# Kernel optimization log

Hardware: AMD Instinct MI355X
Metric: run time of the kernel (lower is better)

Reference implementation:

```python
import jax, jax.numpy as jnp
import numpy as np

S_CONST = float(np.log(9.0))   # self.s = log(9)
K = 1.0                        # soft_sign sharpness (config.k)
RHO = 1.0
ALPHA0 = 0.01
BETA0 = 0.1
DECAY = 0.99


def soft_sign(x, k=K):
    # E2Efold soft sign: sigmoid(2*k*x)
    return jax.nn.sigmoid(2.0 * k * x)


def constraint_matrix(x):
    # x: [B, L, 4] -> m: [B, L, L]; pairing constraint AU+CG+UG outer products,
    # symmetrized, with |i-j|<=3 band zeroed (diags mask in torch version).
    base_a, base_u, base_c, base_g = x[..., 0], x[..., 1], x[..., 2], x[..., 3]

    def sym_outer(p, q):
        m = p[:, :, None] * q[:, None, :]
        return m + jnp.swapaxes(m, -1, -2)

    m = sym_outer(base_a, base_u) + sym_outer(base_c, base_g) + sym_outer(base_u, base_g)
    L = x.shape[1]
    i = jnp.arange(L)
    band = jnp.abs(i[:, None] - i[None, :]) <= 3  # [L, L] bool
    return jnp.where(band, jnp.zeros((), m.dtype), m)


def contact_a(a_hat, m):
    a = a_hat * a_hat
    a = (a + jnp.swapaxes(a, -1, -2)) * 0.5
    return a * m


def setup_inputs() -> dict:
    key = jax.random.key(0)
    k1, k2 = jax.random.split(key)
    B, L = 16, 512
    u = jax.random.normal(k1, (B, L, L), jnp.float32) * 2.0
    x = jax.random.uniform(k2, (B, L, 4), jnp.float32)
    return {"u": u, "x": x, "timesteps": 20}


def reference(u, x, timesteps):
    m = constraint_matrix(x)
    u = soft_sign(u - S_CONST) * u
    a_hat = jax.nn.sigmoid(u) * jax.lax.stop_gradient(soft_sign(u - S_CONST))
    a = contact_a(a_hat, m)
    lmbd = jax.lax.stop_gradient(jax.nn.relu(jnp.sum(a, -1) - 1.0))

    # per-step decayed learning rates: step t uses alpha0*decay^t (for grad step)
    # and alpha0*decay^(t+1) for the soft-threshold (torch decays alpha in between)
    t_idx = jnp.arange(timesteps, dtype=jnp.float32)
    alphas = ALPHA0 * DECAY ** t_idx
    betas = BETA0 * DECAY ** t_idx

    def step(carry, ab):
        lmbd, a, a_hat = carry
        alpha, beta = ab
        grad_a = -u / 2.0 + (lmbd * soft_sign(jnp.sum(a, -1) - 1.0))[..., None]
        grad = a_hat * m * (grad_a + jnp.swapaxes(grad_a, -1, -2))
        a_hat_new = a_hat - alpha * grad
        a_hat_new = jax.nn.relu(jnp.abs(a_hat_new) - RHO * alpha * DECAY)
        a_hat_new = jnp.clip(a_hat_new, -1.0, 1.0)
        a_new = contact_a(a_hat_new, m)
        lmbd_new = lmbd + beta * jax.nn.relu(jnp.sum(a_new, -1) - 1.0)
        return (lmbd_new, a_new, a_hat_new), a_new

    _, a_stack = jax.lax.scan(step, (lmbd, a, a_hat), (alphas, betas))
    return a_stack  # [timesteps, B, L, L] == a_t_list[1:]
```

## Files before the change

### kernel.cpp

```cpp
#include <hip/hip_runtime.h>
#include <math.h>

#define BB 16
#define LL 512
#define TS 20
#define TT 64
#define NT (LL / TT)
#define NPAIR (NT * (NT + 1) / 2)
#define NUNIT 32
#define NBLK (BB * NUNIT)
#define BLL (BB * LL * LL)
#define NROW (BB * LL)
#define RSPSTEP (BB * NT * LL)
#define PADI 32

#define S_CONST 2.19722457733621938f

__device__ __forceinline__ float sgm(float v) { return 1.0f / (1.0f + __expf(-v)); }
__device__ __forceinline__ float ahat_of(float up) {
  return sgm(up) * sgm(2.0f * (up - S_CONST));
}

__device__ __forceinline__ void st_agent(float* p, float v) {
  __hip_atomic_store(p, v, __ATOMIC_RELAXED, __HIP_MEMORY_SCOPE_AGENT);
}
__device__ __forceinline__ float ld_agent(const float* p) {
  return __hip_atomic_load(p, __ATOMIC_RELAXED, __HIP_MEMORY_SCOPE_AGENT);
}
__device__ __forceinline__ void bump(int* p) {
  __hip_atomic_fetch_add(p, 1, __ATOMIC_RELAXED, __HIP_MEMORY_SCOPE_AGENT);
}
__device__ __forceinline__ void spin_ge(const int* p, int target) {
  while (__hip_atomic_load(p, __ATOMIC_RELAXED, __HIP_MEMORY_SCOPE_AGENT) < target) {
    __builtin_amdgcn_s_sleep(1);
  }
  asm volatile("" ::: "memory");
}

__device__ __forceinline__ void decode_unit(int p, int& RI, int& RJ, bool& dg) {
  if (p < 28) {
    int base = 0, i = 0;
    while (p >= base + (NT - 1 - i)) { base += NT - 1 - i; ++i; }
    RI = i;
    RJ = i + 1 + (p - base);
    dg = false;
  } else {
    int g = p - 28;
    RI = 2 * g;
    RJ = 2 * g + 1;
    dg = true;
  }
}

__global__ __launch_bounds__(256, 2) void k_fused(const float* __restrict__ u,
                                                  const float* __restrict__ x,
                                                  float* __restrict__ rsp,
                                                  int* __restrict__ arr,
                                                  float* __restrict__ out) {
  __shared__ float t1[TT][TT + 1];
  __shared__ float t2[TT][TT + 1];
  __shared__ float xr[2][TT][4];
  __shared__ float xt[2][TT][4];
  __shared__ float cI[TT];
  __shared__ float cJ[TT];

  int b = blockIdx.x / NUNIT;
  int p = blockIdx.x % NUNIT;
  int RI, RJ;
  bool dg;
  decode_unit(p, RI, RJ, dg);
  int C1 = dg ? RI : RJ;
  int C2 = dg ? RJ : RI;

  int tid = threadIdx.x;
  int tx = tid & 15, ty = tid >> 4;

  int* ctrI = &arr[(b * NT + RI) * PADI];
  int* ctrJ = &arr[(b * NT + RJ) * PADI];

  if (tid < 128) {
    int which = tid >> 6;
    int r = tid & 63;
    int gi = (which ? RJ : RI) * TT + r;
    const float* xp = x + ((b * LL) + gi) * 4;
    float A = xp[0], U = xp[1], C = xp[2], G = xp[3];
    xr[which][r][0] = A; xr[which][r][1] = U; xr[which][r][2] = C; xr[which][r][3] = G;
    xt[which][r][0] = U; xt[which][r][1] = A + G; xt[which][r][2] = G; xt[which][r][3] = C + U;
  }

  int lrow = 0;
  if (tid < 128) {
    int which = tid >> 6;
    int r = tid & 63;
    lrow = (which ? RJ : RI) * TT + r;
  }
  float lmbd = 0.0f;

  float av1[4][4], av2[4][4];
  float wv1[4][4], wv2[4][4];
  float mv1[4][4], mv2[4][4];

  __syncthreads();

#pragma unroll
  for (int k = 0; k < 4; ++k) {
    int r = ty + 16 * k;
    {
      int i = RI * TT + r;
      int off = (b * LL + i) * LL + C1 * TT + 4 * tx;
      float4 u4 = *reinterpret_cast<const float4*>(u + off);
      float uu[4] = {u4.x, u4.y, u4.z, u4.w};
#pragma unroll
      for (int q = 0; q < 4; ++q) {
        float up = sgm(2.0f * (uu[q] - S_CONST)) * uu[q];
        t1[r][4 * tx + q] = up;
        av1[k][q] = ahat_of(up);
      }
    }
    {
      int i = RJ * TT + r;
      int off = (b * LL + i) * LL + C2 * TT + 4 * tx;
      float4 u4 = *reinterpret_cast<const float4*>(u + off);
      float uu[4] = {u4.x, u4.y, u4.z, u4.w};
#pragma unroll
      for (int q = 0; q < 4; ++q) {
        float up = sgm(2.0f * (uu[q] - S_CONST)) * uu[q];
        t2[r][4 * tx + q] = up;
        av2[k][q] = ahat_of(up);
      }
    }
  }
  __syncthreads();

  {
    float (*T1)[TT + 1] = dg ? t1 : t2;
    float (*T2)[TT + 1] = dg ? t2 : t1;
    float (*xc1)[4] = dg ? xt[0] : xt[1];
    float (*xc2)[4] = dg ? xt[1] : xt[0];
    float* rsp0 = rsp;

#pragma unroll
    for (int k = 0; k < 4; ++k) {
      int r = ty + 16 * k;
      {
        int i = RI * TT + r;
        float rs = 0.0f;
#pragma unroll
        for (int q = 0; q < 4; ++q) {
          int c = 4 * tx + q;
          int j = C1 * TT + c;
          float upT = T1[c][r];
          wv1[k][q] = -0.5f * (t1[r][c] + upT);
          int d = i - j; d = d < 0 ? -d : d;
          float mm = (d <= 3) ? 0.0f
                              : xr[0][r][0] * xc1[c][0] + xr[0][r][1] * xc1[c][1] +
                                    xr[0][r][2] * xc1[c][2] + xr[0][r][3] * xc1[c][3];
          mv1[k][q] = mm;
          float aT = ahat_of(upT);
          float a = av1[k][q];
          rs += 0.5f * (a * a + aT * aT) * mm;
        }
        rs += __shfl_xor(rs, 1); rs += __shfl_xor(rs, 2);
        rs += __shfl_xor(rs, 4); rs += __shfl_xor(rs, 8);
        if (tx == 0) st_agent(&rsp0[(b * NT + C1) * LL + i], rs);
      }
      {
        int i = RJ * TT + r;
        float rs = 0.0f;
#pragma unroll
        for (int q = 0; q < 4; ++q) {
          int c = 4 * tx + q;
          int j = C2 * TT + c;
          float upT = T2[c][r];
          wv2[k][q] = -0.5f * (t2[r][c] + upT);
          int d = i - j; d = d < 0 ? -d : d;
          float mm = (d <= 3) ? 0.0f
                              : xr[1][r][0] * xc2[c][0] + xr[1][r][1] * xc2[c][1] +
                                    xr[1][r][2] * xc2[c][2] + xr[1][r][3] * xc2[c][3];
          mv2[k][q] = mm;
          float aT = ahat_of(upT);
          float a = av2[k][q];
          rs += 0.5f * (a * a + aT * aT) * mm;
        }
        rs += __shfl_xor(rs, 1); rs += __shfl_xor(rs, 2);
        rs += __shfl_xor(rs, 4); rs += __shfl_xor(rs, 8);
        if (tx == 0) st_agent(&rsp0[(b * NT + C2) * LL + i], rs);
      }
    }
  }

  __builtin_amdgcn_s_waitcnt(0);
  __syncthreads();
  if (tid == 0) bump(ctrI);
  if (tid == 64) bump(ctrJ);

  float alpha = 0.01f;
  float beta_prev = 0.0f;

  for (int t = 0; t < TS; ++t) {
    if (tid == 0) spin_ge(ctrI, 8 * (t + 1));
    if (tid == 64) spin_ge(ctrJ, 8 * (t + 1));
    __syncthreads();

    if (tid < 128) {
      const float* rp = rsp + (size_t)t * RSPSTEP + b * NT * LL + lrow;
      float rsv = 0.0f;
#pragma unroll
      for (int ct = 0; ct < NT; ++ct) rsv += ld_agent(rp + ct * LL);
      float dv = rsv - 1.0f;
      float rel = dv > 0.0f ? dv : 0.0f;
      lmbd = (t == 0) ? rel : lmbd + beta_prev * rel;
      float cv = lmbd * sgm(2.0f * dv);
      if (tid >= 64) cJ[tid & 63] = cv; else cI[tid] = cv;
    }
    __syncthreads();

    float thr = alpha * 0.99f;
    float* cc1 = dg ? cI : cJ;
    float* cc2 = dg ? cJ : cI;

#pragma unroll
    for (int k = 0; k < 4; ++k) {
      int r = ty + 16 * k;
      {
        float ci = cI[r];
#pragma unroll
        for (int q = 0; q < 4; ++q) {
          int c = 4 * tx + q;
          float a = av1[k][q];
          float g = a * mv1[k][q] * (wv1[k][q] + ci + cc1[c]);
          float an = a - alpha * g;
          an = fabsf(an) - thr;
          an = an > 0.0f ? an : 0.0f;
          an = an < 1.0f ? an : 1.0f;
          av1[k][q] = an;
          t1[r][c] = an;
        }
      }
      {
        float ci = cJ[r];
#pragma unroll
        for (int q = 0; q < 4; ++q) {
          int c = 4 * tx + q;
          float a = av2[k][q];
          float g = a * mv2[k][q] * (wv2[k][q] + ci + cc2[c]);
          float an = a - alpha * g;
          an = fabsf(an) - thr;
          an = an > 0.0f ? an : 0.0f;
          an = an < 1.0f ? an : 1.0f;
          av2[k][q] = an;
          t2[r][c] = an;
        }
      }
    }
    __syncthreads();

    float (*T1)[TT + 1] = dg ? t1 : t2;
    float (*T2)[TT + 1] = dg ? t2 : t1;
    float* op = out + (size_t)t * BLL;
    float* rs_next = rsp + (size_t)(t + 1) * RSPSTEP;
#pragma unroll
    for (int k = 0; k < 4; ++k) {
      int r = ty + 16 * k;
      {
        int i = RI * TT + r;
        int off = (b * LL + i) * LL + C1 * TT + 4 * tx;
        float res[4];
        float rs = 0.0f;
#pragma unroll
        for (int q = 0; q < 4; ++q) {
          int c = 4 * tx + q;
          float a = av1[k][q];
          float bt = T1[c][r];
          float v = 0.5f * (a * a + bt * bt) * mv1[k][q];
          res[q] = v;
          rs += v;
        }
        rs += __shfl_xor(rs, 1); rs += __shfl_xor(rs, 2);
        rs += __shfl_xor(rs, 4); rs += __shfl_xor(rs, 8);
        if (tx == 0) st_agent(&rs_next[(b * NT + C1) * LL + i], rs);
        *reinterpret_cast<float4*>(op + off) = make_float4(res[0], res[1], res[2], res[3]);
      }
      {
        int i = RJ * TT + r;
        int off = (b * LL + i) * LL + C2 * TT + 4 * tx;
        float res[4];
        float rs = 0.0f;
#pragma unroll
        for (int q = 0; q < 4; ++q) {
          int c = 4 * tx + q;
          float a = av2[k][q];
          float bt = T2[c][r];
          float v = 0.5f * (a * a + bt * bt) * mv2[k][q];
          res[q] = v;
          rs += v;
        }
        rs += __shfl_xor(rs, 1); rs += __shfl_xor(rs, 2);
        rs += __shfl_xor(rs, 4); rs += __shfl_xor(rs, 8);
        if (tx == 0) st_agent(&rs_next[(b * NT + C2) * LL + i], rs);
        *reinterpret_cast<float4*>(op + off) = make_float4(res[0], res[1], res[2], res[3]);
      }
    }

    __builtin_amdgcn_s_waitcnt(0);
    __syncthreads();
    if (t != TS - 1) {
      if (tid == 0) bump(ctrI);
      if (tid == 64) bump(ctrJ);
    }

    beta_prev = (t == 0) ? 0.1f : beta_prev * 0.99f;
    alpha *= 0.99f;
  }
}

__device__ __forceinline__ void decode_pair(int p, int& I, int& J) {
  int base = 0, i = 0;
  while (p >= base + (NT - i)) { base += NT - i; ++i; }
  I = i;
  J = i + (p - base);
}

__global__ __launch_bounds__(256) void k_init(const float* __restrict__ u,
                                              const float* __restrict__ x,
                                              float* __restrict__ w,
                                              float* __restrict__ ah,
                                              float* __restrict__ rowsum) {
  __shared__ float up1[TT][TT + 1];
  __shared__ float up2[TT][TT + 1];
  __shared__ float xr[2][TT][4];
  __shared__ float xt[2][TT][4];

  int b = blockIdx.x / NPAIR;
  int p = blockIdx.x % NPAIR;
  int I, J;
  decode_pair(p, I, J);
  bool diag = (I == J);
  int tid = threadIdx.x;
  int tx = tid & 15, ty = tid >> 4;

  if (tid < 128) {
    int which = tid >> 6;
    int r = tid & 63;
    int gi = (which ? J : I) * TT + r;
    const float* xp = x + ((b * LL) + gi) * 4;
    float A = xp[0], U = xp[1], C = xp[2], G = xp[3];
    xr[which][r][0] = A; xr[which][r][1] = U; xr[which][r][2] = C; xr[which][r][3] = G;
    xt[which][r][0] = U; xt[which][r][1] = A + G; xt[which][r][2] = G; xt[which][r][3] = C + U;
  }

  float a1r[4][4], a2r[4][4];

#pragma unroll
  for (int k = 0; k < 4; ++k) {
    int r = ty + 16 * k;
    {
      int i = I * TT + r;
      int off = (b * LL + i) * LL + J * TT + 4 * tx;
      float4 u4 = *reinterpret_cast<const float4*>(u + off);
      float uu[4] = {u4.x, u4.y, u4.z, u4.w};
      float av[4];
#pragma unroll
      for (int q = 0; q < 4; ++q) {
        float up = sgm(2.0f * (uu[q] - S_CONST)) * uu[q];
        up1[r][4 * tx + q] = up;
        av[q] = ahat_of(up);
        a1r[k][q] = av[q];
      }
      *reinterpret_cast<float4*>(ah + off) = make_float4(av[0], av[1], av[2], av[3]);
    }
    if (!diag) {
      int i = J * TT + r;
      int off = (b * LL + i) * LL + I * TT + 4 * tx;
      float4 u4 = *reinterpret_cast<const float4*>(u + off);
      float uu[4] = {u4.x, u4.y, u4.z, u4.w};
      float av[4];
#pragma unroll
      for (int q = 0; q < 4; ++q) {
        float up = sgm(2.0f * (uu[q] - S_CONST)) * uu[q];
        up2[r][4 * tx + q] = up;
        av[q] = ahat_of(up);
        a2r[k][q] = av[q];
      }
      *reinterpret_cast<float4*>(ah + off) = make_float4(av[0], av[1], av[2], av[3]);
    }
  }
  __syncthreads();

  float (*U2)[TT + 1] = diag ? up1 : up2;

#pragma unroll
  for (int k = 0; k < 4; ++k) {
    int r = ty + 16 * k;
    {
      int i = I * TT + r;
      int off = (b * LL + i) * LL + J * TT + 4 * tx;
      float wv[4];
      float rs = 0.0f;
#pragma unroll
      for (int q = 0; q < 4; ++q) {
        int c = 4 * tx + q;
        int j = J * TT + c;
        float upT = U2[c][r];
        wv[q] = -0.5f * (up1[r][c] + upT);
        int d = i - j; d = d < 0 ? -d : d;
        float mm = (d <= 3) ? 0.0f
                            : xr[0][r][0] * xt[1][c][0] + xr[0][r][1] * xt[1][c][1] +
                                  xr[0][r][2] * xt[1][c][2] + xr[0][r][3] * xt[1][c][3];
        float aT = ahat_of(upT);
        float a = a1r[k][q];
        rs += 0.5f * (a * a + aT * aT) * mm;
      }
      *reinterpret_cast<float4*>(w + off) = make_float4(wv[0], wv[1], wv[2], wv[3]);
      rs += __shfl_xor(rs, 1); rs += __shfl_xor(rs, 2);
      rs += __shfl_xor(rs, 4); rs += __shfl_xor(rs, 8);
      if (tx == 0) atomicAdd(&rowsum[b * LL + i], rs);
    }
    if (!diag) {
      int i = J * TT + r;
      int off = (b * LL + i) * LL + I * TT + 4 * tx;
      float wv[4];
      float rs = 0.0f;
#pragma unroll
      for (int q = 0; q < 4; ++q) {
        int c = 4 * tx + q;
        int j = I * TT + c;
        float upT = up1[c][r];
        wv[q] = -0.5f * (up2[r][c] + upT);
        int d = i - j; d = d < 0 ? -d : d;
        float mm = (d <= 3) ? 0.0f
                            : xr[1][r][0] * xt[0][c][0] + xr[1][r][1] * xt[0][c][1] +
                                  xr[1][r][2] * xt[0][c][2] + xr[1][r][3] * xt[0][c][3];
        float aT = ahat_of(upT);
        float a = a2r[k][q];
        rs += 0.5f * (a * a + aT * aT) * mm;
      }
      *reinterpret_cast<float4*>(w + off) = make_float4(wv[0], wv[1], wv[2], wv[3]);
      rs += __shfl_xor(rs, 1); rs += __shfl_xor(rs, 2);
      rs += __shfl_xor(rs, 4); rs += __shfl_xor(rs, 8);
      if (tx == 0) atomicAdd(&rowsum[b * LL + i], rs);
    }
  }
}

__global__ __launch_bounds__(256) void k_c(float* __restrict__ lmbd,
                                           const float* __restrict__ rs,
                                           float* __restrict__ cc,
                                           float* __restrict__ rsn,
                                           float beta_prev, int first) {
  int idx = blockIdx.x * blockDim.x + threadIdx.x;
  if (idx >= NROW) return;
  float t = rs[idx] - 1.0f;
  float rel = t > 0.0f ? t : 0.0f;
  float l = first ? rel : lmbd[idx] + beta_prev * rel;
  lmbd[idx] = l;
  cc[idx] = l * sgm(2.0f * t);
  rsn[idx] = 0.0f;
}

__global__ __launch_bounds__(256) void k_step(const float* __restrict__ x,
                                              const float* __restrict__ w,
                                              float* __restrict__ ah,
                                              const float* __restrict__ cvec,
                                              float* __restrict__ rsn,
                                              float* __restrict__ out,
                                              float alpha, float thr) {
  __shared__ float an1[TT][TT + 1];
  __shared__ float an2[TT][TT + 1];
  __shared__ float xr[2][TT][4];
  __shared__ float xt[2][TT][4];
  __shared__ float cI[TT];
  __shared__ float cJ[TT];

  int b = blockIdx.x / NPAIR;
  int p = blockIdx.x % NPAIR;
  int I, J;
  decode_pair(p, I, J);
  bool diag = (I == J);
  int tid = threadIdx.x;
  int tx = tid & 15, ty = tid >> 4;

  if (tid < 128) {
    int which = tid >> 6;
    int r = tid & 63;
    int gi = (which ? J : I) * TT + r;
    const float* xp = x + ((b * LL) + gi) * 4;
    float A = xp[0], U = xp[1], C = xp[2], G = xp[3];
    xr[which][r][0] = A; xr[which][r][1] = U; xr[which][r][2] = C; xr[which][r][3] = G;
    xt[which][r][0] = U; xt[which][r][1] = A + G; xt[which][r][2] = G; xt[which][r][3] = C + U;
  } else {
    int t2i = tid - 128;
    int which = t2i >> 6;
    int r = t2i & 63;
    int gi = (which ? J : I) * TT + r;
    float cv = cvec[b * LL + gi];
    if (which) cJ[r] = cv; else cI[r] = cv;
  }
  __syncthreads();

  float m1[4][4], m2[4][4];

#pragma unroll
  for (int k = 0; k < 4; ++k) {
    int r = ty + 16 * k;
    {
      int i = I * TT + r;
      int off = (b * LL + i) * LL + J * TT + 4 * tx;
      float4 a4 = *reinterpret_cast<const float4*>(ah + off);
      float4 w4 = *reinterpret_cast<const float4*>(w + off);
      float av[4] = {a4.x, a4.y, a4.z, a4.w};
      float wv[4] = {w4.x, w4.y, w4.z, w4.w};
      float ci = cI[r];
      float res[4];
#pragma unroll
      for (int q = 0; q < 4; ++q) {
        int c = 4 * tx + q;
        int j = J * TT + c;
        int d = i - j; d = d < 0 ? -d : d;
        float mm = (d <= 3) ? 0.0f
                            : xr[0][r][0] * xt[1][c][0] + xr[0][r][1] * xt[1][c][1] +
                                  xr[0][r][2] * xt[1][c][2] + xr[0][r][3] * xt[1][c][3];
        m1[k][q] = mm;
        float g = av[q] * mm * (wv[q] + ci + cJ[c]);
        float an = av[q] - alpha * g;
        an = fabsf(an) - thr;
        an = an > 0.0f ? an : 0.0f;
        an = an < 1.0f ? an : 1.0f;
        res[q] = an;
        an1[r][c] = an;
      }
      *reinterpret_cast<float4*>(ah + off) = make_float4(res[0], res[1], res[2], res[3]);
    }
    if (!diag) {
      int i = J * TT + r;
      int off = (b * LL + i) * LL + I * TT + 4 * tx;
      float4 a4 = *reinterpret_cast<const float4*>(ah + off);
      float4 w4 = *reinterpret_cast<const float4*>(w + off);
      float av[4] = {a4.x, a4.y, a4.z, a4.w};
      float wv[4] = {w4.x, w4.y, w4.z, w4.w};
      float ci = cJ[r];
      float res[4];
#pragma unroll
      for (int q = 0; q < 4; ++q) {
        int c = 4 * tx + q;
        int j = I * TT + c;
        int d = i - j; d = d < 0 ? -d : d;
        float mm = (d <= 3) ? 0.0f
                            : xr[1][r][0] * xt[0][c][0] + xr[1][r][1] * xt[0][c][1] +
                                  xr[1][r][2] * xt[0][c][2] + xr[1][r][3] * xt[0][c][3];
        m2[k][q] = mm;
        float g = av[q] * mm * (wv[q] + ci + cI[c]);
        float an = av[q] - alpha * g;
        an = fabsf(an) - thr;
        an = an > 0.0f ? an : 0.0f;
        an = an < 1.0f ? an : 1.0f;
        res[q] = an;
        an2[r][c] = an;
      }
      *reinterpret_cast<float4*>(ah + off) = make_float4(res[0], res[1], res[2], res[3]);
    }
  }
  __syncthreads();

  float (*A2)[TT + 1] = diag ? an1 : an2;

#pragma unroll
  for (int k = 0; k < 4; ++k) {
    int r = ty + 16 * k;
    {
      int i = I * TT + r;
      int off = (b * LL + i) * LL + J * TT + 4 * tx;
      float res[4];
      float rs = 0.0f;
#pragma unroll
      for (int q = 0; q < 4; ++q) {
        int c = 4 * tx + q;
        float a = an1[r][c];
        float bt = A2[c][r];
        float v = 0.5f * (a * a + bt * bt) * m1[k][q];
        res[q] = v;
        rs += v;
      }
      *reinterpret_cast<float4*>(out + off) = make_float4(res[0], res[1], res[2], res[3]);
      rs += __shfl_xor(rs, 1); rs += __shfl_xor(rs, 2);
      rs += __shfl_xor(rs, 4); rs += __shfl_xor(rs, 8);
      if (tx == 0) atomicAdd(&rsn[b * LL + i], rs);
    }
    if (!diag) {
      int i = J * TT + r;
      int off = (b * LL + i) * LL + I * TT + 4 * tx;
      float res[4];
      float rs = 0.0f;
#pragma unroll
      for (int q = 0; q < 4; ++q) {
        int c = 4 * tx + q;
        float a = an2[r][c];
        float bt = an1[c][r];
        float v = 0.5f * (a * a + bt * bt) * m2[k][q];
        res[q] = v;
        rs += v;
      }
      *reinterpret_cast<float4*>(out + off) = make_float4(res[0], res[1], res[2], res[3]);
      rs += __shfl_xor(rs, 1); rs += __shfl_xor(rs, 2);
      rs += __shfl_xor(rs, 4); rs += __shfl_xor(rs, 8);
      if (tx == 0) atomicAdd(&rsn[b * LL + i], rs);
    }
  }
}

extern "C" void kernel_launch(void* const* d_in, const int* in_sizes, int n_in,
                              void* d_out, int out_size, void* d_ws, size_t ws_size,
                              hipStream_t stream) {
  const float* u = (const float*)d_in[0];
  const float* x = (const float*)d_in[1];
  float* out = (float*)d_out;
  float* ws = (float*)d_ws;

  float* rsp = ws;
  int* arr = (int*)(ws + (size_t)(TS + 1) * RSPSTEP);
  hipMemsetAsync(arr, 0, BB * NT * PADI * sizeof(int), stream);

  void* args[] = {(void*)&u, (void*)&x, (void*)&rsp, (void*)&arr, (void*)&out};
  hipError_t err = hipLaunchCooperativeKernel((void*)k_fused, dim3(NBLK),
                                              dim3(256), args, 0, stream);
  if (err == hipSuccess) return;

  float* w = ws;
  float* ah = ws + (size_t)BLL;
  float* rsA = ws + 2 * (size_t)BLL;
  float* rsB = rsA + NROW;
  float* cc = rsB + NROW;
  float* lmbd = cc + NROW;

  hipMemsetAsync(rsA, 0, NROW * sizeof(float), stream);

  dim3 grid(BB * NPAIR);
  dim3 block(256);
  k_init<<<grid, block, 0, stream>>>(u, x, w, ah, rsA);

  float* ra = rsA;
  float* rb = rsB;
  for (int t = 0; t < TS; ++t) {
    float alpha = 0.01f * powf(0.99f, (float)t);
    float beta_prev = (t > 0) ? 0.1f * powf(0.99f, (float)(t - 1)) : 0.0f;
    k_c<<<dim3((NROW + 255) / 256), block, 0, stream>>>(lmbd, ra, cc, rb, beta_prev,
                                                        t == 0 ? 1 : 0);
    k_step<<<grid, block, 0, stream>>>(x, w, ah, cc, rb, out + (size_t)t * BLL, alpha,
                                       alpha * 0.99f);
    float* tmp = ra; ra = rb; rb = tmp;
  }
}
```

Before: 446.6 us.

## Publish row sums before output stores to release dependent blocks earlier

Row sums for the next step are now computed right after the a_hat update. Each row sum adds a row partial and column partials from shared memory, using the symmetry of a. The sums are stored and the neighbour counters bumped before the large output write, so other blocks can start the next timestep while this block is still storing a. This shortens the critical path of the cross-block synchronisation. The cost is extra shared memory, an extra barrier, and a reassociated summation order.

```diff
diff --git a/kernel.cpp b/kernel.cpp
--- a/kernel.cpp
+++ b/kernel.cpp
@@ -59,6 +59,10 @@
                                                   float* __restrict__ out) {
   __shared__ float t1[TT][TT + 1];
   __shared__ float t2[TT][TT + 1];
+  __shared__ float colp1[16][TT];
+  __shared__ float colp2[16][TT];
+  __shared__ float rp1[TT];
+  __shared__ float rp2[TT];
   __shared__ float xr[2][TT][4];
   __shared__ float xt[2][TT][4];
   __shared__ float cI[TT];
@@ -218,12 +222,16 @@
     float thr = alpha * 0.99f;
     float* cc1 = dg ? cI : cJ;
     float* cc2 = dg ? cJ : cI;
-
+    bool last = (t == TS - 1);
+
+    float cp1[4] = {0.f, 0.f, 0.f, 0.f};
+    float cp2[4] = {0.f, 0.f, 0.f, 0.f};
 #pragma unroll
     for (int k = 0; k < 4; ++k) {
       int r = ty + 16 * k;
       {
         float ci = cI[r];
+        float rsv = 0.0f;
 #pragma unroll
         for (int q = 0; q < 4; ++q) {
           int c = 4 * tx + q;
@@ -235,10 +243,17 @@
           an = an < 1.0f ? an : 1.0f;
           av1[k][q] = an;
           t1[r][c] = an;
+          float v = 0.5f * an * an * mv1[k][q];
+          rsv += v;
+          cp1[q] += v;
         }
+        rsv += __shfl_xor(rsv, 1); rsv += __shfl_xor(rsv, 2);
+        rsv += __shfl_xor(rsv, 4); rsv += __shfl_xor(rsv, 8);
+        if (tx == 0) rp1[r] = rsv;
       }
       {
         float ci = cJ[r];
+        float rsv = 0.0f;
 #pragma unroll
         for (int q = 0; q < 4; ++q) {
           int c = 4 * tx + q;
@@ -250,15 +265,48 @@
           an = an < 1.0f ? an : 1.0f;
           av2[k][q] = an;
           t2[r][c] = an;
+          float v = 0.5f * an * an * mv2[k][q];
+          rsv += v;
+          cp2[q] += v;
         }
-      }
+        rsv += __shfl_xor(rsv, 1); rsv += __shfl_xor(rsv, 2);
+        rsv += __shfl_xor(rsv, 4); rsv += __shfl_xor(rsv, 8);
+        if (tx == 0) rp2[r] = rsv;
+      }
+    }
+#pragma unroll
+    for (int q = 0; q < 4; ++q) {
+      colp1[ty][4 * tx + q] = cp1[q];
+      colp2[ty][4 * tx + q] = cp2[q];
     }
     __syncthreads();
+
+    if (!last) {
+      float* rs_next = rsp + (size_t)(t + 1) * RSPSTEP;
+      if (tid < 64) {
+        int i = tid;
+        float vsum = rp1[i];
+        float (*cpA)[TT] = dg ? colp1 : colp2;
+#pragma unroll
+        for (int y = 0; y < 16; ++y) vsum += cpA[y][i];
+        st_agent(&rs_next[(b * NT + C1) * LL + RI * TT + i], vsum);
+      } else if (tid < 128) {
+        int i = tid - 64;
+        float vsum = rp2[i];
+        float (*cpB)[TT] = dg ? colp2 : colp1;
+#pragma unroll
+        for (int y = 0; y < 16; ++y) vsum += cpB[y][i];
+        st_agent(&rs_next[(b * NT + C2) * LL + RJ * TT + i], vsum);
+      }
+      __builtin_amdgcn_s_waitcnt(0);
+      __syncthreads();
+      if (tid == 0) bump(ctrI);
+      if (tid == 64) bump(ctrJ);
+    }
 
     float (*T1)[TT + 1] = dg ? t1 : t2;
     float (*T2)[TT + 1] = dg ? t2 : t1;
     float* op = out + (size_t)t * BLL;
-    float* rs_next = rsp + (size_t)(t + 1) * RSPSTEP;
 #pragma unroll
     for (int k = 0; k < 4; ++k) {
       int r = ty + 16 * k;
@@ -266,47 +314,28 @@
         int i = RI * TT + r;
         int off = (b * LL + i) * LL + C1 * TT + 4 * tx;
         float res[4];
-        float rs = 0.0f;
 #pragma unroll
         for (int q = 0; q < 4; ++q) {
           int c = 4 * tx + q;
           float a = av1[k][q];
           float bt = T1[c][r];
-          float v = 0.5f * (a * a + bt * bt) * mv1[k][q];
-          res[q] = v;
-          rs += v;
+          res[q] = 0.5f * (a * a + bt * bt) * mv1[k][q];
         }
-        rs += __shfl_xor(rs, 1); rs += __shfl_xor(rs, 2);
-        rs += __shfl_xor(rs, 4); rs += __shfl_xor(rs, 8);
-        if (tx == 0) st_agent(&rs_next[(b * NT + C1) * LL + i], rs);
         *reinterpret_cast<float4*>(op + off) = make_float4(res[0], res[1], res[2], res[3]);
       }
       {
         int i = RJ * TT + r;
         int off = (b * LL + i) * LL + C2 * TT + 4 * tx;
         float res[4];
-        float rs = 0.0f;
 #pragma unroll
         for (int q = 0; q < 4; ++q) {
           int c = 4 * tx + q;
           float a = av2[k][q];
           float bt = T2[c][r];
-          float v = 0.5f * (a * a + bt * bt) * mv2[k][q];
-          res[q] = v;
-          rs += v;
+          res[q] = 0.5f * (a * a + bt * bt) * mv2[k][q];
         }
-        rs += __shfl_xor(rs, 1); rs += __shfl_xor(rs, 2);
-        rs += __shfl_xor(rs, 4); rs += __shfl_xor(rs, 8);
-        if (tx == 0) st_agent(&rs_next[(b * NT + C2) * LL + i], rs);
         *reinterpret_cast<float4*>(op + off) = make_float4(res[0], res[1], res[2], res[3]);
       }
-    }
-
-    __builtin_amdgcn_s_waitcnt(0);
-    __syncthreads();
-    if (t != TS - 1) {
-      if (tid == 0) bump(ctrI);
-      if (tid == 64) bump(ctrJ);
     }
 
     beta_prev = (t == 0) ? 0.1f : beta_prev * 0.99f;
```

After: 414.5 us. 7.2% less time.
